# Optimization experiments

Hardware: AMD Instinct MI355X
Metric: run time of the kernel (lower is better)

## Reference

```python
import jax, jax.numpy as jnp
import numpy as np

HEADS = 8
DIM_HEAD = 64
SCALE = DIM_HEAD ** -0.5


def setup_inputs() -> dict:
    key = jax.random.key(0)
    ks = jax.random.split(key, 7)
    B, N, M, D, INNER = 2, 4096, 4096, 1024, HEADS * DIM_HEAD
    x = jax.random.normal(ks[0], (B, N, D), dtype=jnp.float32)
    context = jax.random.normal(ks[1], (B, M, D), dtype=jnp.float32)
    Wq = jax.random.normal(ks[2], (D, INNER), dtype=jnp.float32) * 0.02
    Wk = jax.random.normal(ks[3], (D, INNER), dtype=jnp.float32) * 0.02
    Wv = jax.random.normal(ks[4], (D, INNER), dtype=jnp.float32) * 0.02
    Wo = jax.random.normal(ks[5], (INNER, D), dtype=jnp.float32) * 0.02
    bo = jnp.zeros((D,), dtype=jnp.float32)
    return {"x": x, "context": context, "Wq": Wq, "Wk": Wk, "Wv": Wv, "Wo": Wo, "bo": bo}


def reference(x, context, Wq, Wk, Wv, Wo, bo):
    B, N, _ = x.shape
    M = context.shape[1]
    # projections (no bias, as in to_q/to_k/to_v)
    q = (x @ Wq).reshape(B, N, HEADS, DIM_HEAD)        # b n h d
    k = (context @ Wk).reshape(B, M, HEADS, DIM_HEAD)  # b m h d
    v = (context @ Wv).reshape(B, M, HEADS, DIM_HEAD)
    # scaled dot-product attention (the chunk loop in the original is math-equivalent)
    scores = jnp.einsum('bnhd,bmhd->bhnm', q, k) * SCALE
    attn = jax.nn.softmax(scores, axis=-1)
    out = jnp.einsum('bhnm,bmhd->bnhd', attn, v).reshape(B, N, HEADS * DIM_HEAD)
    # to_out: Linear with bias (dropout p=0.0 -> identity)
    return out @ Wo + bo
```

## Files before the change

### kernel.cpp

```cpp
#include <hip/hip_runtime.h>
#include <hip/hip_bf16.h>

typedef short bf16x8 __attribute__((ext_vector_type(8)));
typedef float f32x4 __attribute__((ext_vector_type(4)));
typedef float f32x16 __attribute__((ext_vector_type(16)));

#define MFMA16(a, b, c) __builtin_amdgcn_mfma_f32_16x16x32_bf16((a), (b), (c), 0, 0, 0)
#define MFMA32(a, b, c) __builtin_amdgcn_mfma_f32_32x32x16_bf16((a), (b), (c), 0, 0, 0)

#if __has_builtin(__builtin_amdgcn_exp2f)
#define EXP2(x) __builtin_amdgcn_exp2f(x)
#else
#define EXP2(x) __expf((x) * 0.6931471805599453f)
#endif

__device__ __forceinline__ ushort f2bf(float f) {
  union { float f; unsigned u; } x; x.f = f;
  unsigned u = x.u;
  return (ushort)((u + 0x7fffu + ((u >> 16) & 1u)) >> 16);
}

__device__ __forceinline__ ushort4 pack4(float a, float b, float c, float d) {
  ushort4 w; w.x = f2bf(a); w.y = f2bf(b); w.z = f2bf(c); w.w = f2bf(d); return w;
}

__device__ __forceinline__ unsigned cvtpk(float a, float b) {
  unsigned r;
  asm("v_cvt_pk_bf16_f32 %0, %1, %2" : "=v"(r) : "v"(a), "v"(b));
  return r;
}

__device__ __forceinline__ void plswap(unsigned& a, unsigned& b) {
  asm volatile("v_permlane32_swap_b32 %0, %1" : "+v"(a), "+v"(b));
}

__device__ __forceinline__ float bfbits2f(unsigned hw) {
  union { unsigned u; float f; } x; x.u = hw << 16; return x.f;
}

__device__ __forceinline__ void gl2lds16(const ushort* g, ushort* l) {
  typedef const __attribute__((address_space(1))) unsigned int* gp_t;
  typedef __attribute__((address_space(3))) unsigned int* lp_t;
  __builtin_amdgcn_global_load_lds((gp_t)(const void*)g, (lp_t)(void*)l, 16, 0, 0);
}

__global__ void transpose_cvt64(const float* __restrict__ src, ushort* __restrict__ dst,
                                int R, int C, float scale) {
  __shared__ float t[64][65];
  const int r0 = blockIdx.y * 64, c0 = blockIdx.x * 64;
  const int tid = threadIdx.x;
#pragma unroll
  for (int i = 0; i < 16; i++) {
    int idx = i * 256 + tid; int rr = idx >> 6, cc = idx & 63;
    t[rr][cc] = src[(size_t)(r0 + rr) * C + c0 + cc];
  }
  __syncthreads();
#pragma unroll
  for (int i = 0; i < 16; i++) {
    int idx = i * 256 + tid; int cc = idx >> 6, rr = idx & 63;
    dst[(size_t)(c0 + cc) * R + r0 + rr] = f2bf(t[rr][cc] * scale);
  }
}

__global__ void cvt_f32_bf16(const float* __restrict__ src, ushort* __restrict__ dst, int n8) {
  for (int i = blockIdx.x * 256 + threadIdx.x; i < n8; i += gridDim.x * 256) {
    float4 a = ((const float4*)src)[i * 2];
    float4 b = ((const float4*)src)[i * 2 + 1];
    ((ushort4*)dst)[i * 2]     = pack4(a.x, a.y, a.z, a.w);
    ((ushort4*)dst)[i * 2 + 1] = pack4(b.x, b.y, b.z, b.w);
  }
}

template<int OUT>
__device__ __forceinline__ void gemm_core(ushort* lA, ushort* lB,
                                          const ushort* __restrict__ A,
                                          const ushort* __restrict__ Bt,
                                          void* __restrict__ Cv,
                                          const float* __restrict__ bias,
                                          int N, int K, int row0, int col0) {
  const int tid = threadIdx.x;
  const int lane = tid & 63, wid = tid >> 6;
  const int lr = lane >> 3;
  const int c0 = ((lane & 7) ^ lr) << 3;
  const int wm = (wid >> 1) * 64, wn = (wid & 1) * 64;
  const int lo = lane & 15, hi = lane >> 4;

  const ushort* ga[4]; const ushort* gb[4];
#pragma unroll
  for (int i = 0; i < 4; i++) {
    int g = i * 4 + wid;
    ga[i] = A  + (size_t)(row0 + g * 8 + lr) * K + c0;
    gb[i] = Bt + (size_t)(col0 + g * 8 + lr) * K + c0;
  }

  f32x4 acc[4][4] = {};

  for (int k0 = 0; k0 < K; k0 += 64) {
#pragma unroll
    for (int i = 0; i < 4; i++) {
      int g = i * 4 + wid;
      gl2lds16(ga[i], &lA[g * 512]); ga[i] += 64;
      gl2lds16(gb[i], &lB[g * 512]); gb[i] += 64;
    }
    __syncthreads();
#pragma unroll
    for (int kk = 0; kk < 2; kk++) {
      bf16x8 af[4], bfr[4];
      const int kbyte = kk * 64 + hi * 16;
#pragma unroll
      for (int i = 0; i < 4; i++) {
        int r = wm + i * 16 + lo;
        af[i] = *(const bf16x8*)((const char*)lA + r * 128 + (kbyte ^ ((r & 7) << 4)));
        int c = wn + i * 16 + lo;
        bfr[i] = *(const bf16x8*)((const char*)lB + c * 128 + (kbyte ^ ((c & 7) << 4)));
      }
#pragma unroll
      for (int i = 0; i < 4; i++)
#pragma unroll
        for (int j = 0; j < 4; j++)
          acc[i][j] = MFMA16(af[i], bfr[j], acc[i][j]);
    }
    __syncthreads();
  }

#pragma unroll
  for (int i = 0; i < 4; i++)
#pragma unroll
    for (int j = 0; j < 4; j++)
#pragma unroll
      for (int r = 0; r < 4; r++) {
        int row = row0 + wm + i * 16 + hi * 4 + r;
        int col = col0 + wn + j * 16 + lo;
        float v = acc[i][j][r];
        if (OUT == 1)
          ((float*)Cv)[(size_t)row * N + col] = v + (bias ? bias[col] : 0.f);
        else if (OUT == 0)
          ((ushort*)Cv)[(size_t)row * N + col] = f2bf(v);
        else
          ((ushort*)Cv)[((size_t)(col >> 12) * 512 + row) * 4096 + (col & 4095)] = f2bf(v);
      }
}

__global__ __launch_bounds__(256, 3)
void proj_fused(const ushort* __restrict__ xb, const ushort* __restrict__ ctxb,
                const ushort* __restrict__ Wqt, const ushort* __restrict__ Wkt,
                const ushort* __restrict__ Wvt,
                ushort* __restrict__ Qb, ushort* __restrict__ Kb, ushort* __restrict__ Vtb) {
  __shared__ __align__(16) ushort lA[128 * 64];
  __shared__ __align__(16) ushort lB[128 * 64];
  const int bid = blockIdx.x;
  if (bid < 512) {
    const ushort* A  = bid < 256 ? xb  : ctxb;
    const ushort* Bt = bid < 256 ? Wqt : Wkt;
    ushort* C        = bid < 256 ? Qb  : Kb;
    const int l = bid & 255;
    gemm_core<0>(lA, lB, A, Bt, C, nullptr, 512, 1024, (l & 63) * 128, (l >> 6) * 128);
  } else {
    const int l = bid - 512;
    gemm_core<2>(lA, lB, Wvt, ctxb, Vtb, nullptr, 8192, 1024, (l & 3) * 128, (l >> 2) * 128);
  }
}

__global__ __launch_bounds__(256, 3)
void out_gemm(const ushort* __restrict__ Ob, const ushort* __restrict__ Wot,
              float* __restrict__ out, const float* __restrict__ bo) {
  __shared__ __align__(16) ushort lA[128 * 64];
  __shared__ __align__(16) ushort lB[128 * 64];
  gemm_core<1>(lA, lB, Ob, Wot, out, bo, 1024, 512, blockIdx.x * 128, blockIdx.y * 128);
}

__global__ __launch_bounds__(256, 4)
void attn_kernel(const ushort* __restrict__ Q, const ushort* __restrict__ Kp,
                 const ushort* __restrict__ Vt, unsigned* __restrict__ Opart,
                 float* __restrict__ Lpart) {
  __shared__ __align__(16) ushort kbuf[2][64 * 64];
  __shared__ __align__(16) ushort vbuf[2][64 * 64];

  const int tid = threadIdx.x;
  const int lane = tid & 63, wid = tid >> 6;
  const int bid = blockIdx.x;
  const int kvh = bid >> 9;
  const int b9 = bid & 511;
  const int bh = (b9 & 7) * 2 + (b9 >> 8);
  const int qblk = (b9 >> 3) & 31;
  const int b = bh >> 3, h = bh & 7;
  const int l31 = lane & 31, hi5 = lane >> 5;
  const int qrow = qblk * 128 + wid * 32 + l31;
  const size_t rowbase = (size_t)b * 4096;
  const int hoff = h * 64;
  const int kv0 = kvh * 1024;
  const int swzk = (l31 & 7) << 4;

  bf16x8 qf[4];
  {
    const ushort* qp = Q + (rowbase + qrow) * 512 + hoff + hi5 * 8;
    qf[0] = *(const bf16x8*)(qp);
    qf[1] = *(const bf16x8*)(qp + 16);
    qf[2] = *(const bf16x8*)(qp + 32);
    qf[3] = *(const bf16x8*)(qp + 48);
  }

  const int r0 = wid * 16 + (lane >> 3);
  const int r1 = r0 + 8;
  const int c00 = ((((lane & 7) * 16) ^ ((r0 & 7) << 4)) >> 1);
  const int c01 = ((((lane & 7) * 16) ^ ((r1 & 7) << 4)) >> 1);
  const ushort* kp0 = Kp + (rowbase + kv0 + r0) * 512 + hoff + c00;
  const ushort* kp1 = Kp + (rowbase + kv0 + r1) * 512 + hoff + c01;
  const ushort* vp0 = Vt + ((size_t)bh * 64 + r0) * 4096 + kv0 + c00;
  const ushort* vp1 = Vt + ((size_t)bh * 64 + r1) * 4096 + kv0 + c01;

  float l_run = 0.f;
  f32x16 o0 = {}, o1 = {};

  gl2lds16(kp0, &kbuf[0][wid * 1024]);
  gl2lds16(kp1, &kbuf[0][wid * 1024 + 512]);
  gl2lds16(vp0, &vbuf[0][wid * 1024]);
  gl2lds16(vp1, &vbuf[0][wid * 1024 + 512]);
  __syncthreads();

  for (int t = 0; t < 16; t++) {
    const int cur = t & 1;
    if (t < 15) {
      const size_t ko = (size_t)(t + 1) * (64 * 512);
      const int vo = (t + 1) * 64;
      gl2lds16(kp0 + ko, &kbuf[cur ^ 1][wid * 1024]);
      gl2lds16(kp1 + ko, &kbuf[cur ^ 1][wid * 1024 + 512]);
      gl2lds16(vp0 + vo, &vbuf[cur ^ 1][wid * 1024]);
      gl2lds16(vp1 + vo, &vbuf[cur ^ 1][wid * 1024 + 512]);
    }
    const char* kb = (const char*)kbuf[cur];
    const char* vb = (const char*)vbuf[cur];

    f32x16 s0 = {}, s1 = {};
    __builtin_amdgcn_s_setprio(1);
#pragma unroll
    for (int kt = 0; kt < 4; kt++) {
      bf16x8 kf = *(const bf16x8*)(kb + l31 * 128 + ((kt * 32 + hi5 * 16) ^ swzk));
      s0 = MFMA32(kf, qf[kt], s0);
    }
#pragma unroll
    for (int kt = 0; kt < 4; kt++) {
      bf16x8 kf = *(const bf16x8*)(kb + (32 + l31) * 128 + ((kt * 32 + hi5 * 16) ^ swzk));
      s1 = MFMA32(kf, qf[kt], s1);
    }
    __builtin_amdgcn_s_setprio(0);

#pragma unroll
    for (int i = 0; i < 16; i++) { s0[i] = EXP2(s0[i]); s1[i] = EXP2(s1[i]); }

    float sm[16];
#pragma unroll
    for (int i = 0; i < 8; i++) sm[i] = s0[2 * i] + s0[2 * i + 1];
#pragma unroll
    for (int i = 0; i < 8; i++) sm[8 + i] = s1[2 * i] + s1[2 * i + 1];
#pragma unroll
    for (int st = 8; st > 0; st >>= 1)
#pragma unroll
      for (int i = 0; i < st; i++) sm[i] = sm[2 * i] + sm[2 * i + 1];
    float rs = sm[0];
    rs += __shfl_xor(rs, 32);
    l_run += rs;

    unsigned p0[8], p1[8];
#pragma unroll
    for (int p = 0; p < 8; p++) {
      p0[p] = cvtpk(s0[2 * p], s0[2 * p + 1]);
      p1[p] = cvtpk(s1[2 * p], s1[2 * p + 1]);
    }
    plswap(p0[0], p0[2]); plswap(p0[1], p0[3]);
    plswap(p0[4], p0[6]); plswap(p0[5], p0[7]);
    plswap(p1[0], p1[2]); plswap(p1[1], p1[3]);
    plswap(p1[4], p1[6]); plswap(p1[5], p1[7]);

    union PF { unsigned u[4]; bf16x8 v; } pf[4];
    pf[0].u[0] = p0[0]; pf[0].u[1] = p0[1]; pf[0].u[2] = p0[2]; pf[0].u[3] = p0[3];
    pf[1].u[0] = p0[4]; pf[1].u[1] = p0[5]; pf[1].u[2] = p0[6]; pf[1].u[3] = p0[7];
    pf[2].u[0] = p1[0]; pf[2].u[1] = p1[1]; pf[2].u[2] = p1[2]; pf[2].u[3] = p1[3];
    pf[3].u[0] = p1[4]; pf[3].u[1] = p1[5]; pf[3].u[2] = p1[6]; pf[3].u[3] = p1[7];

    __builtin_amdgcn_s_setprio(1);
#pragma unroll
    for (int ks = 0; ks < 4; ks++) {
      bf16x8 v0 = *(const bf16x8*)(vb + l31 * 128 + ((ks * 32 + hi5 * 16) ^ swzk));
      bf16x8 v1 = *(const bf16x8*)(vb + (32 + l31) * 128 + ((ks * 32 + hi5 * 16) ^ swzk));
      o0 = MFMA32(v0, pf[ks].v, o0);
      o1 = MFMA32(v1, pf[ks].v, o1);
    }
    __builtin_amdgcn_s_setprio(0);

    __syncthreads();
  }

  const float inv = 1.0f / l_run;
  unsigned* op = Opart + ((size_t)kvh * 65536 + (size_t)bh * 4096 + qrow) * 32;
#pragma unroll
  for (int p = 0; p < 8; p++) {
    const int sl = (p & 1) + 4 * (p >> 1) + 2 * hi5;
    op[sl]      = cvtpk(o0[2 * p] * inv, o0[2 * p + 1] * inv);
    op[16 + sl] = cvtpk(o1[2 * p] * inv, o1[2 * p + 1] * inv);
  }
  if (hi5 == 0)
    Lpart[(size_t)kvh * 65536 + (size_t)bh * 4096 + qrow] = l_run;
}

__global__ __launch_bounds__(256)
void attn_merge(const unsigned* __restrict__ Opart, const float* __restrict__ Lpart,
                ushort* __restrict__ Ob) {
  const int idx = blockIdx.x * 256 + threadIdx.x;
  const int qg = idx >> 5, slot = idx & 31;
  float l0 = Lpart[qg];
  float l1 = Lpart[65536 + qg];
  float l2 = Lpart[2 * 65536 + qg];
  float l3 = Lpart[3 * 65536 + qg];
  const float inv = 1.0f / (l0 + l1 + l2 + l3);
  float ra = 0.f, rb = 0.f;
#pragma unroll
  for (int i = 0; i < 4; i++) {
    const float w = (i == 0 ? l0 : i == 1 ? l1 : i == 2 ? l2 : l3) * inv;
    const unsigned u = Opart[((size_t)i * 65536 + qg) * 32 + slot];
    ra += bfbits2f(u & 0xffffu) * w;
    rb += bfbits2f(u >> 16) * w;
  }
  const int dt = slot >> 4, r = slot & 15;
  const int d0 = dt * 32 + 2 * (r & 1) + 8 * (r >> 2) + 4 * ((r >> 1) & 1);
  const int bh = qg >> 12, qrow = qg & 4095;
  unsigned* dst = (unsigned*)(Ob + ((size_t)(bh >> 3) * 4096 + qrow) * 512 + (bh & 7) * 64 + d0);
  *dst = cvtpk(ra, rb);
}

extern "C" void kernel_launch(void* const* d_in, const int* in_sizes, int n_in,
                              void* d_out, int out_size, void* d_ws, size_t ws_size,
                              hipStream_t stream) {
  (void)in_sizes; (void)n_in; (void)out_size;
  const float* x   = (const float*)d_in[0];
  const float* ctx = (const float*)d_in[1];
  const float* Wq  = (const float*)d_in[2];
  const float* Wk  = (const float*)d_in[3];
  const float* Wv  = (const float*)d_in[4];
  const float* Wo  = (const float*)d_in[5];
  const float* bo  = (const float*)d_in[6];

  const float QSCALE = 0.125f * 1.4426950408889634f;
  const size_t MB = 1024 * 1024;
  if (ws_size < 72 * MB) return;
  char* ws = (char*)d_ws;
  ushort* Wqt = (ushort*)(ws + 0 * MB);
  ushort* Wkt = (ushort*)(ws + 1 * MB);
  ushort* Wvt = (ushort*)(ws + 2 * MB);
  ushort* Wot = (ushort*)(ws + 3 * MB);
  ushort* xb   = (ushort*)(ws + 4 * MB);
  ushort* ctxb = (ushort*)(ws + 20 * MB);
  ushort* Qb   = (ushort*)(ws + 40 * MB);
  ushort* Kb   = (ushort*)(ws + 48 * MB);
  ushort* Vtb  = (ushort*)(ws + 56 * MB);
  ushort* Ob   = (ushort*)(ws + 64 * MB);
  unsigned* Opart = (unsigned*)(ws + 4 * MB);
  float*    Lp    = (float*)(ws + 38 * MB);

  transpose_cvt64<<<dim3(8, 16), dim3(256), 0, stream>>>(Wq, Wqt, 1024, 512, QSCALE);
  transpose_cvt64<<<dim3(8, 16), dim3(256), 0, stream>>>(Wk, Wkt, 1024, 512, 1.0f);
  transpose_cvt64<<<dim3(8, 16), dim3(256), 0, stream>>>(Wv, Wvt, 1024, 512, 1.0f);
  transpose_cvt64<<<dim3(16, 8), dim3(256), 0, stream>>>(Wo, Wot, 512, 1024, 1.0f);

  cvt_f32_bf16<<<dim3(2048), dim3(256), 0, stream>>>(x,   xb,   8192 * 1024 / 8);
  cvt_f32_bf16<<<dim3(2048), dim3(256), 0, stream>>>(ctx, ctxb, 8192 * 1024 / 8);

  proj_fused<<<dim3(768), dim3(256), 0, stream>>>(xb, ctxb, Wqt, Wkt, Wvt, Qb, Kb, Vtb);

  attn_kernel<<<dim3(2048), dim3(256), 0, stream>>>(Qb, Kb, Vtb, Opart, Lp);
  attn_merge<<<dim3(8192), dim3(256), 0, stream>>>(Opart, Lp, Ob);

  out_gemm<<<dim3(64, 8), dim3(256), 0, stream>>>(Ob, Wot, (float*)d_out, bo);
}
```

Baseline: 182.3 us.

## Fuse fp32-to-bf16 activation conversion into projection GEMM loads; merge QKV weight transposes

Removes the standalone cvt_f32_bf16 kernels for x and context. The projection GEMM now reads fp32 activations directly, converts them to bf16 in registers with v_cvt_pk_bf16_f32, and writes them into swizzled LDS. The three Q/K/V weight-transpose launches are merged into one launch over a z-grid. This saves two launches and the round trip of bf16 activation copies through memory. In exchange, each projection tile reads fp32 data (twice the bytes) through register-staged loads instead of async global_load_lds, and context is re-read by both the K and V tiles.

New measurement: 167.9 us. 7.9% less time.

```diff
diff --git a/kernel.cpp b/kernel.cpp
--- a/kernel.cpp
+++ b/kernel.cpp
@@ -20,10 +20,6 @@
   return (ushort)((u + 0x7fffu + ((u >> 16) & 1u)) >> 16);
 }
 
-__device__ __forceinline__ ushort4 pack4(float a, float b, float c, float d) {
-  ushort4 w; w.x = f2bf(a); w.y = f2bf(b); w.z = f2bf(c); w.w = f2bf(d); return w;
-}
-
 __device__ __forceinline__ unsigned cvtpk(float a, float b) {
   unsigned r;
   asm("v_cvt_pk_bf16_f32 %0, %1, %2" : "=v"(r) : "v"(a), "v"(b));
@@ -42,6 +38,31 @@
   typedef const __attribute__((address_space(1))) unsigned int* gp_t;
   typedef __attribute__((address_space(3))) unsigned int* lp_t;
   __builtin_amdgcn_global_load_lds((gp_t)(const void*)g, (lp_t)(void*)l, 16, 0, 0);
+}
+
+__global__ void transpose_qkv(const float* __restrict__ Wq, const float* __restrict__ Wk,
+                              const float* __restrict__ Wv, ushort* __restrict__ Wqt,
+                              ushort* __restrict__ Wkt, ushort* __restrict__ Wvt,
+                              float qscale) {
+  __shared__ float t[64][65];
+  const int z = blockIdx.z;
+  const float* src = z == 0 ? Wq : z == 1 ? Wk : Wv;
+  ushort* dst = z == 0 ? Wqt : z == 1 ? Wkt : Wvt;
+  const float scale = z == 0 ? qscale : 1.0f;
+  const int R = 1024, C = 512;
+  const int r0 = blockIdx.y * 64, c0 = blockIdx.x * 64;
+  const int tid = threadIdx.x;
+#pragma unroll
+  for (int i = 0; i < 16; i++) {
+    int idx = i * 256 + tid; int rr = idx >> 6, cc = idx & 63;
+    t[rr][cc] = src[(size_t)(r0 + rr) * C + c0 + cc];
+  }
+  __syncthreads();
+#pragma unroll
+  for (int i = 0; i < 16; i++) {
+    int idx = i * 256 + tid; int cc = idx >> 6, rr = idx & 63;
+    dst[(size_t)(c0 + cc) * R + r0 + rr] = f2bf(t[rr][cc] * scale);
+  }
 }
 
 __global__ void transpose_cvt64(const float* __restrict__ src, ushort* __restrict__ dst,
@@ -62,45 +83,76 @@
   }
 }
 
-__global__ void cvt_f32_bf16(const float* __restrict__ src, ushort* __restrict__ dst, int n8) {
-  for (int i = blockIdx.x * 256 + threadIdx.x; i < n8; i += gridDim.x * 256) {
-    float4 a = ((const float4*)src)[i * 2];
-    float4 b = ((const float4*)src)[i * 2 + 1];
-    ((ushort4*)dst)[i * 2]     = pack4(a.x, a.y, a.z, a.w);
-    ((ushort4*)dst)[i * 2 + 1] = pack4(b.x, b.y, b.z, b.w);
-  }
-}
-
-template<int OUT>
+template<int OUT, int AF32, int BF32>
 __device__ __forceinline__ void gemm_core(ushort* lA, ushort* lB,
-                                          const ushort* __restrict__ A,
-                                          const ushort* __restrict__ Bt,
+                                          const void* __restrict__ Av,
+                                          const void* __restrict__ Bv,
                                           void* __restrict__ Cv,
                                           const float* __restrict__ bias,
                                           int N, int K, int row0, int col0) {
   const int tid = threadIdx.x;
   const int lane = tid & 63, wid = tid >> 6;
   const int lr = lane >> 3;
-  const int c0 = ((lane & 7) ^ lr) << 3;
+  const int cswz = ((lane & 7) ^ lr) << 3;
+  const int clin = (lane & 7) << 3;
+  const int wbyte = (clin * 2) ^ (lr << 4);
   const int wm = (wid >> 1) * 64, wn = (wid & 1) * 64;
   const int lo = lane & 15, hi = lane >> 4;
 
-  const ushort* ga[4]; const ushort* gb[4];
-#pragma unroll
-  for (int i = 0; i < 4; i++) {
-    int g = i * 4 + wid;
-    ga[i] = A  + (size_t)(row0 + g * 8 + lr) * K + c0;
-    gb[i] = Bt + (size_t)(col0 + g * 8 + lr) * K + c0;
-  }
-
   f32x4 acc[4][4] = {};
 
   for (int k0 = 0; k0 < K; k0 += 64) {
-#pragma unroll
-    for (int i = 0; i < 4; i++) {
-      int g = i * 4 + wid;
-      gl2lds16(ga[i], &lA[g * 512]); ga[i] += 64;
-      gl2lds16(gb[i], &lB[g * 512]); gb[i] += 64;
+    if (AF32) {
+      const float* A = (const float*)Av;
+      float4 v0[4], v1[4];
+#pragma unroll
+      for (int i = 0; i < 4; i++) {
+        const float* p = A + (size_t)(row0 + (i * 4 + wid) * 8 + lr) * K + k0 + clin;
+        v0[i] = *(const float4*)p;
+        v1[i] = *(const float4*)(p + 4);
+      }
+#pragma unroll
+      for (int i = 0; i < 4; i++) {
+        uint4 w;
+        w.x = cvtpk(v0[i].x, v0[i].y);
+        w.y = cvtpk(v0[i].z, v0[i].w);
+        w.z = cvtpk(v1[i].x, v1[i].y);
+        w.w = cvtpk(v1[i].z, v1[i].w);
+        *(uint4*)((char*)lA + ((i * 4 + wid) * 8 + lr) * 128 + wbyte) = w;
+      }
+    } else {
+      const ushort* A = (const ushort*)Av;
+#pragma unroll
+      for (int i = 0; i < 4; i++) {
+        int g = i * 4 + wid;
+        gl2lds16(A + (size_t)(row0 + g * 8 + lr) * K + k0 + cswz, &lA[g * 512]);
+      }
+    }
+    if (BF32) {
+      const float* B = (const float*)Bv;
+      float4 v0[4], v1[4];
+#pragma unroll
+      for (int i = 0; i < 4; i++) {
+        const float* p = B + (size_t)(col0 + (i * 4 + wid) * 8 + lr) * K + k0 + clin;
+        v0[i] = *(const float4*)p;
+        v1[i] = *(const float4*)(p + 4);
+      }
+#pragma unroll
+      for (int i = 0; i < 4; i++) {
+        uint4 w;
+        w.x = cvtpk(v0[i].x, v0[i].y);
+        w.y = cvtpk(v0[i].z, v0[i].w);
+        w.z = cvtpk(v1[i].x, v1[i].y);
+        w.w = cvtpk(v1[i].z, v1[i].w);
+        *(uint4*)((char*)lB + ((i * 4 + wid) * 8 + lr) * 128 + wbyte) = w;
+      }
+    } else {
+      const ushort* B = (const ushort*)Bv;
+#pragma unroll
+      for (int i = 0; i < 4; i++) {
+        int g = i * 4 + wid;
+        gl2lds16(B + (size_t)(col0 + g * 8 + lr) * K + k0 + cswz, &lB[g * 512]);
+      }
     }
     __syncthreads();
 #pragma unroll
@@ -142,7 +194,7 @@
 }
 
 __global__ __launch_bounds__(256, 3)
-void proj_fused(const ushort* __restrict__ xb, const ushort* __restrict__ ctxb,
+void proj_fused(const float* __restrict__ x, const float* __restrict__ ctx,
                 const ushort* __restrict__ Wqt, const ushort* __restrict__ Wkt,
                 const ushort* __restrict__ Wvt,
                 ushort* __restrict__ Qb, ushort* __restrict__ Kb, ushort* __restrict__ Vtb) {
@@ -150,14 +202,14 @@
   __shared__ __align__(16) ushort lB[128 * 64];
   const int bid = blockIdx.x;
   if (bid < 512) {
-    const ushort* A  = bid < 256 ? xb  : ctxb;
-    const ushort* Bt = bid < 256 ? Wqt : Wkt;
-    ushort* C        = bid < 256 ? Qb  : Kb;
+    const float* A    = bid < 256 ? x   : ctx;
+    const ushort* Bt  = bid < 256 ? Wqt : Wkt;
+    ushort* C         = bid < 256 ? Qb  : Kb;
     const int l = bid & 255;
-    gemm_core<0>(lA, lB, A, Bt, C, nullptr, 512, 1024, (l & 63) * 128, (l >> 6) * 128);
+    gemm_core<0, 1, 0>(lA, lB, A, Bt, C, nullptr, 512, 1024, (l & 63) * 128, (l >> 6) * 128);
   } else {
     const int l = bid - 512;
-    gemm_core<2>(lA, lB, Wvt, ctxb, Vtb, nullptr, 8192, 1024, (l & 3) * 128, (l >> 2) * 128);
+    gemm_core<2, 0, 1>(lA, lB, Wvt, ctx, Vtb, nullptr, 8192, 1024, (l & 3) * 128, (l >> 2) * 128);
   }
 }
 
@@ -166,7 +218,7 @@
               float* __restrict__ out, const float* __restrict__ bo) {
   __shared__ __align__(16) ushort lA[128 * 64];
   __shared__ __align__(16) ushort lB[128 * 64];
-  gemm_core<1>(lA, lB, Ob, Wot, out, bo, 1024, 512, blockIdx.x * 128, blockIdx.y * 128);
+  gemm_core<1, 0, 0>(lA, lB, Ob, Wot, out, bo, 1024, 512, blockIdx.x * 128, blockIdx.y * 128);
 }
 
 __global__ __launch_bounds__(256, 4)
@@ -348,24 +400,17 @@
   ushort* Wkt = (ushort*)(ws + 1 * MB);
   ushort* Wvt = (ushort*)(ws + 2 * MB);
   ushort* Wot = (ushort*)(ws + 3 * MB);
-  ushort* xb   = (ushort*)(ws + 4 * MB);
-  ushort* ctxb = (ushort*)(ws + 20 * MB);
+  unsigned* Opart = (unsigned*)(ws + 4 * MB);
+  float*    Lp    = (float*)(ws + 38 * MB);
   ushort* Qb   = (ushort*)(ws + 40 * MB);
   ushort* Kb   = (ushort*)(ws + 48 * MB);
   ushort* Vtb  = (ushort*)(ws + 56 * MB);
   ushort* Ob   = (ushort*)(ws + 64 * MB);
-  unsigned* Opart = (unsigned*)(ws + 4 * MB);
-  float*    Lp    = (float*)(ws + 38 * MB);
-
-  transpose_cvt64<<<dim3(8, 16), dim3(256), 0, stream>>>(Wq, Wqt, 1024, 512, QSCALE);
-  transpose_cvt64<<<dim3(8, 16), dim3(256), 0, stream>>>(Wk, Wkt, 1024, 512, 1.0f);
-  transpose_cvt64<<<dim3(8, 16), dim3(256), 0, stream>>>(Wv, Wvt, 1024, 512, 1.0f);
+
+  transpose_qkv<<<dim3(8, 16, 3), dim3(256), 0, stream>>>(Wq, Wk, Wv, Wqt, Wkt, Wvt, QSCALE);
   transpose_cvt64<<<dim3(16, 8), dim3(256), 0, stream>>>(Wo, Wot, 512, 1024, 1.0f);
 
-  cvt_f32_bf16<<<dim3(2048), dim3(256), 0, stream>>>(x,   xb,   8192 * 1024 / 8);
-  cvt_f32_bf16<<<dim3(2048), dim3(256), 0, stream>>>(ctx, ctxb, 8192 * 1024 / 8);
-
-  proj_fused<<<dim3(768), dim3(256), 0, stream>>>(xb, ctxb, Wqt, Wkt, Wvt, Qb, Kb, Vtb);
+  proj_fused<<<dim3(768), dim3(256), 0, stream>>>(x, ctx, Wqt, Wkt, Wvt, Qb, Kb, Vtb);
 
   attn_kernel<<<dim3(2048), dim3(256), 0, stream>>>(Qb, Kb, Vtb, Opart, Lp);
   attn_merge<<<dim3(8192), dim3(256), 0, stream>>>(Opart, Lp, Ob);
```
